# Performance work log

Hardware: AMD Instinct MI355X
Metric: run time of the kernel (lower is better)

Reference implementation:

```python
import jax, jax.numpy as jnp
import numpy as np

NUM_SPECIAL = 3  # rows 1..NUM_SPECIAL in special table; row 0 is padding (zeros)

def setup_inputs() -> dict:
    key = jax.random.key(0)
    ks = jax.random.split(key, 16)
    T, B, E, H, L, V = 128, 32, 512, 512, 2, 32000
    G = 4 * H
    s = 0.02
    special_emb = jax.random.normal(ks[1], (NUM_SPECIAL + 1, E), jnp.float32) * s
    special_emb = special_emb.at[0].set(0.0)  # padding_idx=0
    return {
        "ids": jax.random.randint(ks[0], (T, B), 0, V),
        "length_countdown": jax.random.uniform(ks[2], (T, B, 1), jnp.float32),
        "word_emb": jax.random.normal(ks[3], (V, E), jnp.float32) * s,
        "special_emb": special_emb,
        "h0": jax.random.normal(ks[4], (L, B, H), jnp.float32) * s,
        "c0": jax.random.normal(ks[5], (L, B, H), jnp.float32) * s,
        "prev_output": jnp.zeros((B, H), jnp.float32),
        "Wih0": jax.random.normal(ks[6], (G, E + H + 1), jnp.float32) * s,
        "Whh0": jax.random.normal(ks[7], (G, H), jnp.float32) * s,
        "bih0": jnp.zeros((G,), jnp.float32),
        "bhh0": jnp.zeros((G,), jnp.float32),
        "Wih1": jax.random.normal(ks[8], (G, H), jnp.float32) * s,
        "Whh1": jax.random.normal(ks[9], (G, H), jnp.float32) * s,
        "bih1": jnp.zeros((G,), jnp.float32),
        "bhh1": jnp.zeros((G,), jnp.float32),
        "Wg": jax.random.normal(ks[10], (V, H), jnp.float32) * s,
        "bg": jnp.zeros((V,), jnp.float32),
    }

def _lstm_cell(x, h, c, Wih, Whh, bih, bhh):
    gates = x @ Wih.T + bih + h @ Whh.T + bhh  # [B, 4H]
    i, f, g, o = jnp.split(gates, 4, axis=-1)  # torch LSTMCell gate order
    c_new = jax.nn.sigmoid(f) * c + jax.nn.sigmoid(i) * jnp.tanh(g)
    h_new = jax.nn.sigmoid(o) * jnp.tanh(c_new)
    return h_new, c_new

def reference(ids, length_countdown, word_emb, special_emb, h0, c0, prev_output,
              Wih0, Whh0, bih0, bhh0, Wih1, Whh1, bih1, bhh1, Wg, bg):
    # embeddings = word_embeddings(ids) + special_embeddings(special_ids(ids))
    sp_ids = jnp.where(ids < NUM_SPECIAL, ids + 1, 0)
    emb = word_emb[ids] + special_emb[sp_ids]                 # [T,B,E]
    rnn_in = jnp.concatenate([emb, length_countdown], axis=2)  # [T,B,E+1]

    Wihs = (Wih0, Wih1); Whhs = (Whh0, Whh1)
    bihs = (bih0, bih1); bhhs = (bhh0, bhh1)
    L = h0.shape[0]

    def step(carry, emb_t):
        out, h, c = carry
        x = jnp.concatenate([emb_t, out], axis=1)  # input feeding
        hs, cs = [], []
        for l in range(L):
            h_l, c_l = _lstm_cell(x, h[l], c[l], Wihs[l], Whhs[l], bihs[l], bhhs[l])
            x = h_l  # dropout=0
            hs.append(h_l); cs.append(c_l)
        out = x
        score = jax.nn.log_softmax(out @ Wg.T + bg, axis=-1)  # generator
        return (out, jnp.stack(hs), jnp.stack(cs)), score

    (out, hT, cT), scores = jax.lax.scan(step, (prev_output, h0, c0), rnn_in)
    return scores, (hT, cT), out
```

## Files before the change

kernel.cpp:

```cpp
#include <hip/hip_runtime.h>
#include <hip/hip_bf16.h>


typedef __attribute__((ext_vector_type(8))) short bf16x8;
typedef __attribute__((ext_vector_type(4))) float f32x4;
typedef __attribute__((ext_vector_type(2))) unsigned long long u64x2;

#define AS1 __attribute__((address_space(1)))
#define AS3 __attribute__((address_space(3)))

__device__ __forceinline__ unsigned short f2bf(float f) {
  unsigned int u = __builtin_bit_cast(unsigned int, f);
  u += 0x7fffu + ((u >> 16) & 1u);
  return (unsigned short)(u >> 16);
}

__device__ __forceinline__ void gl16(const void* g, void* l) {
  __builtin_amdgcn_global_load_lds((const AS1 unsigned int*)g,
                                   (AS3 unsigned int*)l, 16, 0, 0);
}

__device__ __forceinline__ float sigm(float x) { return 1.0f / (1.0f + __expf(-x)); }

__global__ __launch_bounds__(256, 1) void prep_k(
    const float* __restrict__ Wg,  const float* __restrict__ Wih0,
    const float* __restrict__ Whh0,const float* __restrict__ Wih1,
    const float* __restrict__ Whh1,const float* __restrict__ bih0,
    const float* __restrict__ bhh0,const float* __restrict__ bih1,
    const float* __restrict__ bhh1,const float* __restrict__ h0,
    const float* __restrict__ pout,
    unsigned short* __restrict__ WgBf, unsigned short* __restrict__ W0e,
    unsigned short* __restrict__ Wr0p, unsigned short* __restrict__ Wr1p,
    float* __restrict__ b1p, float* __restrict__ bias0c,
    float* __restrict__ wcd, unsigned short* __restrict__ H0X,
    unsigned short* __restrict__ FOUT, unsigned short* __restrict__ H1I)
{
  const long N0 = 16384000L;
  const long N1 = N0 + 1048576L;
  const long N2 = N1 + 2097152L;
  const long N3 = N2 + 2097152L;
  const long N4 = N3 + 2048L;
  const long N5 = N4 + 2048L;
  const long N6 = N5 + 2048L;
  const long N7 = N6 + 393216L;
  for (long i = blockIdx.x * 256L + threadIdx.x; i < N7; i += 256L * gridDim.x) {
    if (i < N0) {
      WgBf[i] = f2bf(Wg[i]);
    } else if (i < N1) {
      long k = i - N0; int g = (int)(k >> 9); int kk = (int)(k & 511);
      W0e[k] = f2bf(Wih0[g * 1025 + kk]);
    } else if (i < N2) {
      long k = i - N1; int gp = (int)(k >> 10); int kk = (int)(k & 1023);
      int j = gp >> 2, gate = gp & 3; int g = gate * 512 + j;
      float v = (kk < 512) ? Whh0[g * 512 + kk] : Wih0[g * 1025 + 513 + (kk - 512)];
      Wr0p[k] = f2bf(v);
    } else if (i < N3) {
      long k = i - N2; int gp = (int)(k >> 10); int kk = (int)(k & 1023);
      int j = gp >> 2, gate = gp & 3; int g = gate * 512 + j;
      float v = (kk < 512) ? Wih1[g * 512 + kk] : Whh1[g * 512 + (kk - 512)];
      Wr1p[k] = f2bf(v);
    } else if (i < N4) {
      int gp = (int)(i - N3); int j = gp >> 2, gate = gp & 3; int g = gate * 512 + j;
      b1p[gp] = bih1[g] + bhh1[g];
    } else if (i < N5) {
      int g = (int)(i - N4); bias0c[g] = bih0[g] + bhh0[g];
    } else if (i < N6) {
      int g = (int)(i - N5); wcd[g] = Wih0[g * 1025 + 512];
    } else {
      long k = i - N6;
      int sub = (int)(k / 131072L);
      int e = (int)(k - (long)sub * 131072L);
      int e2 = e & 16383;
      int wgx = e2 >> 9, b = (e2 >> 4) & 31, jl = e2 & 15;
      int j = wgx * 16 + jl;
      float v = (sub == 0) ? h0[b * 512 + j]
              : (sub == 1) ? h0[16384 + b * 512 + j]
                           : pout[b * 512 + j];
      unsigned short* dst = (sub == 0) ? H0X : (sub == 1) ? H1I : FOUT;
      dst[e] = f2bf(v);
    }
  }
}

__global__ __launch_bounds__(256, 1) void emb_k(
    const int* __restrict__ ids, const float* __restrict__ wemb,
    const float* __restrict__ semb, unsigned short* __restrict__ ebf)
{
  const int tb = blockIdx.x;
  const int id = ids[tb];
  const int sp = (id < 3) ? (id + 1) : 0;
  const float* wr = wemb + (long)id * 512;
  const float* sr = semb + sp * 512;
  for (int i = threadIdx.x; i < 512; i += 256)
    ebf[tb * 512 + i] = f2bf(wr[i] + sr[i]);
}

template<int EPI>
__global__ __launch_bounds__(256, 1) void gemm_bt(
    const unsigned short* __restrict__ A,
    const unsigned short* __restrict__ B, int N,
    float* __restrict__ C,
    const float* __restrict__ e0, const float* __restrict__ e1,
    const float* __restrict__ e2)
{
  __shared__ unsigned short sA[4096];
  __shared__ unsigned short sB[4096];
  const int tid = threadIdx.x;
  const int l = tid & 63, w = tid >> 6;
  const int nb = N >> 7;
  const int bid = blockIdx.x;
  const int bm = bid / nb, bn = bid - bm * nb;

  const int u0 = w * 128 + l;
  const int u1 = u0 + 64;
  const int r0 = u0 >> 2, c0 = (u0 & 3) ^ (r0 & 3);
  const int r1 = u1 >> 2, c1 = (u1 & 3) ^ (r1 & 3);
  const unsigned short* ga0 = A + (long)(bm * 128 + r0) * 512 + c0 * 8;
  const unsigned short* ga1 = A + (long)(bm * 128 + r1) * 512 + c1 * 8;
  const unsigned short* gb0 = B + (long)(bn * 128 + r0) * 512 + c0 * 8;
  const unsigned short* gb1 = B + (long)(bn * 128 + r1) * 512 + c1 * 8;
  unsigned short* la0 = sA + (w * 2 + 0) * 512;
  unsigned short* la1 = sA + (w * 2 + 1) * 512;
  unsigned short* lb0 = sB + (w * 2 + 0) * 512;
  unsigned short* lb1 = sB + (w * 2 + 1) * 512;

  const int fr = l & 15, fc = l >> 4;
  const int wm = w >> 1, wn = w & 1;
  int aoff[4], boff[4];
#pragma unroll
  for (int mi = 0; mi < 4; ++mi) {
    int row = wm * 64 + mi * 16 + fr;
    aoff[mi] = row * 64 + ((fc ^ (row & 3)) * 16);
  }
#pragma unroll
  for (int ni = 0; ni < 4; ++ni) {
    int row = wn * 64 + ni * 16 + fr;
    boff[ni] = row * 64 + ((fc ^ (row & 3)) * 16);
  }

  f32x4 acc[4][4];
#pragma unroll
  for (int i = 0; i < 4; ++i)
#pragma unroll
    for (int jq = 0; jq < 4; ++jq) acc[i][jq] = (f32x4){0.f, 0.f, 0.f, 0.f};

  for (int kt = 0; kt < 16; ++kt) {
    __syncthreads();
    gl16(ga0 + kt * 32, la0);
    gl16(ga1 + kt * 32, la1);
    gl16(gb0 + kt * 32, lb0);
    gl16(gb1 + kt * 32, lb1);
    asm volatile("s_waitcnt vmcnt(0)" ::: "memory");
    __syncthreads();
    bf16x8 av[4], bv[4];
#pragma unroll
    for (int mi = 0; mi < 4; ++mi)
      av[mi] = *(const bf16x8*)((const char*)sA + aoff[mi]);
#pragma unroll
    for (int ni = 0; ni < 4; ++ni)
      bv[ni] = *(const bf16x8*)((const char*)sB + boff[ni]);
#pragma unroll
    for (int mi = 0; mi < 4; ++mi)
#pragma unroll
      for (int ni = 0; ni < 4; ++ni)
        acc[mi][ni] = __builtin_amdgcn_mfma_f32_16x16x32_bf16(av[mi], bv[ni], acc[mi][ni], 0, 0, 0);
  }

  const int mbase = bm * 128 + wm * 64;
  const int nbase = bn * 128 + wn * 64;
#pragma unroll
  for (int mi = 0; mi < 4; ++mi)
#pragma unroll
    for (int ni = 0; ni < 4; ++ni) {
      const int col = nbase + ni * 16 + fr;
#pragma unroll
      for (int r = 0; r < 4; ++r) {
        const int row = mbase + mi * 16 + fc * 4 + r;
        float v = acc[mi][ni][r];
        if (EPI == 0) {
          const int gp = ((row & 511) << 2) | (row >> 9);
          v += e0[row] + e2[col] * e1[row];
          C[(long)gp * N + col] = v;
        } else {
          v += e0[col];
          C[(long)row * N + col] = v;
        }
      }
    }
}

__global__ __launch_bounds__(256, 1) void lstm_seq(
    const unsigned short* __restrict__ Wr0p,
    const unsigned short* __restrict__ Wr1p,
    const float* __restrict__ P0t, const float* __restrict__ b1p,
    const float* __restrict__ c0in,
    unsigned short* __restrict__ H0X, unsigned short* __restrict__ H1X,
    const unsigned short* __restrict__ FOUT, const unsigned short* __restrict__ H1I,
    unsigned short* __restrict__ outbf, float* __restrict__ outs,
    unsigned int* __restrict__ flagA, unsigned int* __restrict__ flagB)
{
  const int tid = threadIdx.x;
  const int wg = blockIdx.x;
  const int l = tid & 63, w = tid >> 6;
  const int fr = l & 15, fc = l >> 4;

  __shared__ unsigned short sx[32768];
  __shared__ float sg[32][65];
  __shared__ unsigned short sh[32][16];

  unsigned int xcc;
  asm("s_getreg_b32 %0, hwreg(HW_REG_XCC_ID)" : "=s"(xcc));
  const int eoff = (int)(xcc & 7) << 14;
  const int foff = (int)(xcc & 7) << 10;

  const int b = tid & 31, jl0 = tid >> 5;
  const int sb = l >> 1, sjh = l & 1;

  float c0r[2], c1r[2], h0k[2], h1k[2];
#pragma unroll
  for (int jq = 0; jq < 2; ++jq) {
    c0r[jq] = c0in[b * 512 + wg * 16 + jl0 + jq * 8];
    c1r[jq] = c0in[16384 + b * 512 + wg * 16 + jl0 + jq * 8];
    h0k[jq] = 0.f; h1k[jq] = 0.f;
  }

  float b1v[8];
#pragma unroll
  for (int jq = 0; jq < 2; ++jq)
#pragma unroll
    for (int g = 0; g < 4; ++g)
      b1v[jq * 4 + g] = b1p[(wg * 16 + jl0 + jq * 8) * 4 + g];

  const char* sxb0 = (const char*)sx + fr * 2048;
  const char* sxb1 = (const char*)sx + (16 + fr) * 2048;
  const int xr = (fr & 7) << 4;
  const int wrow = (wg * 64 + w * 16 + fr) * 1024 + fc * 8;

  char* const sxw = (char*)sx + sb * 2048;
  const int sswz = (sb & 7) << 4;

#define STAGE2(srcp, half)                                                    \
  do {                                                                        \
    unsigned long long q0[8], q1[8];                                          \
    _Pragma("unroll")                                                         \
    for (int i = 0; i < 8; ++i) {                                             \
      int u = i * 256 + tid;                                                  \
      q0[i] = __hip_atomic_load((const unsigned long long*)((srcp) + eoff) + u * 2, \
                                __ATOMIC_RELAXED, __HIP_MEMORY_SCOPE_AGENT);  \
      q1[i] = __hip_atomic_load((const unsigned long long*)((srcp) + eoff) + u * 2 + 1, \
                                __ATOMIC_RELAXED, __HIP_MEMORY_SCOPE_AGENT);  \
    }                                                                         \
    _Pragma("unroll")                                                         \
    for (int i = 0; i < 8; ++i) {                                             \
      int cb = (half) * 1024 + (i * 4 + w) * 32 + sjh * 16;                   \
      u64x2 v; v.x = q0[i]; v.y = q1[i];                                      \
      *(u64x2*)(sxw + (cb ^ sswz)) = v;                                       \
    }                                                                         \
  } while (0)

#define MFMA_HALF(Wp, k0, e0v, o0v, e1v, o1v)                                 \
  do {                                                                        \
    _Pragma("unroll")                                                         \
    for (int kp = 0; kp < 8; ++kp) {                                          \
      int kta = (k0) + kp * 2, ktb = kta + 1;                                 \
      bf16x8 bva = *(const bf16x8*)((Wp) + wrow + kta * 32);                  \
      bf16x8 x0a = *(const bf16x8*)(sxb0 + ((kta * 64 + fc * 16) ^ xr));      \
      bf16x8 x1a = *(const bf16x8*)(sxb1 + ((kta * 64 + fc * 16) ^ xr));      \
      e0v = __builtin_amdgcn_mfma_f32_16x16x32_bf16(x0a, bva, e0v, 0, 0, 0);  \
      e1v = __builtin_amdgcn_mfma_f32_16x16x32_bf16(x1a, bva, e1v, 0, 0, 0);  \
      bf16x8 bvb = *(const bf16x8*)((Wp) + wrow + ktb * 32);                  \
      bf16x8 x0b = *(const bf16x8*)(sxb0 + ((ktb * 64 + fc * 16) ^ xr));      \
      bf16x8 x1b = *(const bf16x8*)(sxb1 + ((ktb * 64 + fc * 16) ^ xr));      \
      o0v = __builtin_amdgcn_mfma_f32_16x16x32_bf16(x0b, bvb, o0v, 0, 0, 0);  \
      o1v = __builtin_amdgcn_mfma_f32_16x16x32_bf16(x1b, bvb, o1v, 0, 0, 0);  \
    }                                                                         \
  } while (0)

#define POLL(flags, tgt)                                                      \
  do {                                                                        \
    const unsigned int* fp = (flags) + foff + ((l & 31) << 5);                \
    for (;;) {                                                                \
      unsigned int f = __hip_atomic_load(fp, __ATOMIC_RELAXED,                \
                                         __HIP_MEMORY_SCOPE_AGENT);           \
      if (__all((int)(f >= (unsigned int)(tgt)))) break;                      \
      __builtin_amdgcn_s_sleep(1);                                            \
    }                                                                         \
    asm volatile("" ::: "memory");                                            \
  } while (0)

  STAGE2(H0X, 0);
  __syncthreads();
  if (w == 0 && l < 8)
    __hip_atomic_store(&flagB[l * 1024 + (wg << 5)], 1u,
                       __ATOMIC_RELAXED, __HIP_MEMORY_SCOPE_AGENT);

  for (int t = 0; t < 128; ++t) {
    float p0v[8];
#pragma unroll
    for (int jq = 0; jq < 2; ++jq)
#pragma unroll
      for (int g = 0; g < 4; ++g)
        p0v[jq * 4 + g] =
            P0t[(long)((wg * 16 + jl0 + jq * 8) * 4 + g) * 4096 + t * 32 + b];

    f32x4 aA0e = (f32x4){0.f,0.f,0.f,0.f}, aA0o = (f32x4){0.f,0.f,0.f,0.f};
    f32x4 aA1e = (f32x4){0.f,0.f,0.f,0.f}, aA1o = (f32x4){0.f,0.f,0.f,0.f};
    MFMA_HALF(Wr0p, 0, aA0e, aA0o, aA1e, aA1o);

    POLL(flagB, t + 1);
    if (t == 0) STAGE2(FOUT, 1); else STAGE2(H1X, 1);
    __syncthreads();
    MFMA_HALF(Wr0p, 16, aA0e, aA0o, aA1e, aA1o);
    {
      f32x4 s0 = aA0e + aA0o, s1 = aA1e + aA1o;
#pragma unroll
      for (int r = 0; r < 4; ++r) {
        sg[fc * 4 + r][w * 16 + fr] = s0[r];
        sg[16 + fc * 4 + r][w * 16 + fr] = s1[r];
      }
    }
    __syncthreads();
#pragma unroll
    for (int jq = 0; jq < 2; ++jq) {
      const int jl = jl0 + jq * 8;
      float gi = sg[b][jl * 4 + 0] + p0v[jq * 4 + 0];
      float gf = sg[b][jl * 4 + 1] + p0v[jq * 4 + 1];
      float gg = sg[b][jl * 4 + 2] + p0v[jq * 4 + 2];
      float go = sg[b][jl * 4 + 3] + p0v[jq * 4 + 3];
      float cn = sigm(gf) * c0r[jq] + sigm(gi) * tanhf(gg);
      float hn = sigm(go) * tanhf(cn);
      c0r[jq] = cn; h0k[jq] = hn;
      sh[b][jl] = f2bf(hn);
    }
    __syncthreads();
    if (w == 0) {
      u64x2 v = *(const u64x2*)&sh[sb][sjh * 8];
      unsigned long long* dst0 =
          (unsigned long long*)(H0X + wg * 512 + sb * 16 + sjh * 8);
#pragma unroll
      for (int r = 0; r < 8; ++r) {
        __hip_atomic_store(dst0 + r * 2048,     v.x, __ATOMIC_RELAXED, __HIP_MEMORY_SCOPE_AGENT);
        __hip_atomic_store(dst0 + r * 2048 + 1, v.y, __ATOMIC_RELAXED, __HIP_MEMORY_SCOPE_AGENT);
      }
      asm volatile("s_waitcnt vmcnt(0)" ::: "memory");
      if (l < 8)
        __hip_atomic_store(&flagA[l * 1024 + (wg << 5)], (unsigned int)(t + 1),
                           __ATOMIC_RELAXED, __HIP_MEMORY_SCOPE_AGENT);
    }

    f32x4 aB0e = (f32x4){0.f,0.f,0.f,0.f}, aB0o = (f32x4){0.f,0.f,0.f,0.f};
    f32x4 aB1e = (f32x4){0.f,0.f,0.f,0.f}, aB1o = (f32x4){0.f,0.f,0.f,0.f};
    if (t == 0) {
      STAGE2(H1I, 1);
      __syncthreads();
    }
    MFMA_HALF(Wr1p, 16, aB0e, aB0o, aB1e, aB1o);

    POLL(flagA, t + 1);
    STAGE2(H0X, 0);
    __syncthreads();
    MFMA_HALF(Wr1p, 0, aB0e, aB0o, aB1e, aB1o);
    {
      f32x4 s0 = aB0e + aB0o, s1 = aB1e + aB1o;
#pragma unroll
      for (int r = 0; r < 4; ++r) {
        sg[fc * 4 + r][w * 16 + fr] = s0[r];
        sg[16 + fc * 4 + r][w * 16 + fr] = s1[r];
      }
    }
    __syncthreads();
#pragma unroll
    for (int jq = 0; jq < 2; ++jq) {
      const int jl = jl0 + jq * 8;
      float gi = sg[b][jl * 4 + 0] + b1v[jq * 4 + 0];
      float gf = sg[b][jl * 4 + 1] + b1v[jq * 4 + 1];
      float gg = sg[b][jl * 4 + 2] + b1v[jq * 4 + 2];
      float go = sg[b][jl * 4 + 3] + b1v[jq * 4 + 3];
      float cn = sigm(gf) * c1r[jq] + sigm(gi) * tanhf(gg);
      float hn = sigm(go) * tanhf(cn);
      c1r[jq] = cn; h1k[jq] = hn;
      sh[b][jl] = f2bf(hn);
    }
    __syncthreads();
    if (w == 0) {
      u64x2 v = *(const u64x2*)&sh[sb][sjh * 8];
      unsigned long long* dst0 =
          (unsigned long long*)(H1X + wg * 512 + sb * 16 + sjh * 8);
#pragma unroll
      for (int r = 0; r < 8; ++r) {
        __hip_atomic_store(dst0 + r * 2048,     v.x, __ATOMIC_RELAXED, __HIP_MEMORY_SCOPE_AGENT);
        __hip_atomic_store(dst0 + r * 2048 + 1, v.y, __ATOMIC_RELAXED, __HIP_MEMORY_SCOPE_AGENT);
      }
      asm volatile("s_waitcnt vmcnt(0)" ::: "memory");
      if (l < 8)
        __hip_atomic_store(&flagB[l * 1024 + (wg << 5)], (unsigned int)(t + 2),
                           __ATOMIC_RELAXED, __HIP_MEMORY_SCOPE_AGENT);
    } else if (w == 1) {
      u64x2 v = *(const u64x2*)&sh[sb][sjh * 8];
      *(u64x2*)(outbf + (t * 32 + sb) * 512 + wg * 16 + sjh * 8) = v;
    }
  }
#undef STAGE2
#undef MFMA_HALF
#undef POLL

  float* hT = outs + 131072000;
  float* cT = outs + 131072000 + 32768;
  float* oT = outs + 131072000 + 65536;
#pragma unroll
  for (int jq = 0; jq < 2; ++jq) {
    const int j = wg * 16 + jl0 + jq * 8;
    hT[b * 512 + j] = h0k[jq];
    hT[16384 + b * 512 + j] = h1k[jq];
    cT[b * 512 + j] = c0r[jq];
    cT[16384 + b * 512 + j] = c1r[jq];
    oT[b * 512 + j] = h1k[jq];
  }
}

__global__ __launch_bounds__(256, 1) void lse_fix(float* __restrict__ sc)
{
  const long row = blockIdx.x;
  float4* p4 = (float4*)(sc + row * 32000L);
  const int tid = threadIdx.x;
  float m = -3.0e38f, s = 0.0f;
  for (int i = tid; i < 8000; i += 256) {
    float4 v = p4[i];
    float m4 = fmaxf(fmaxf(v.x, v.y), fmaxf(v.z, v.w));
    float mn = fmaxf(m, m4);
    s = s * __expf(m - mn) + __expf(v.x - mn) + __expf(v.y - mn)
        + __expf(v.z - mn) + __expf(v.w - mn);
    m = mn;
  }
#pragma unroll
  for (int off = 32; off > 0; off >>= 1) {
    float mo = __shfl_down(m, off);
    float so = __shfl_down(s, off);
    float mn = fmaxf(m, mo);
    s = s * __expf(m - mn) + so * __expf(mo - mn);
    m = mn;
  }
  __shared__ float lm[4], ls[4], lse_sh;
  if ((tid & 63) == 0) { lm[tid >> 6] = m; ls[tid >> 6] = s; }
  __syncthreads();
  if (tid == 0) {
    float M = lm[0], S = ls[0];
#pragma unroll
    for (int i = 1; i < 4; ++i) {
      float mn = fmaxf(M, lm[i]);
      S = S * __expf(M - mn) + ls[i] * __expf(lm[i] - mn);
      M = mn;
    }
    lse_sh = M + __logf(S);
  }
  __syncthreads();
  const float lse = lse_sh;
  for (int i = tid; i < 8000; i += 256) {
    float4 v = p4[i];
    v.x -= lse; v.y -= lse; v.z -= lse; v.w -= lse;
    p4[i] = v;
  }
}

extern "C" void kernel_launch(void* const* d_in, const int* in_sizes, int n_in,
                              void* d_out, int out_size, void* d_ws, size_t ws_size,
                              hipStream_t stream) {
  const int*   ids  = (const int*)d_in[0];
  const float* cd   = (const float*)d_in[1];
  const float* wemb = (const float*)d_in[2];
  const float* semb = (const float*)d_in[3];
  const float* h0   = (const float*)d_in[4];
  const float* c0   = (const float*)d_in[5];
  const float* pout = (const float*)d_in[6];
  const float* Wih0 = (const float*)d_in[7];
  const float* Whh0 = (const float*)d_in[8];
  const float* bih0 = (const float*)d_in[9];
  const float* bhh0 = (const float*)d_in[10];
  const float* Wih1 = (const float*)d_in[11];
  const float* Whh1 = (const float*)d_in[12];
  const float* bih1 = (const float*)d_in[13];
  const float* bhh1 = (const float*)d_in[14];
  const float* Wg   = (const float*)d_in[15];
  const float* bg   = (const float*)d_in[16];
  float* out = (float*)d_out;

  char* ws = (char*)d_ws;
  unsigned short* WgBf   = (unsigned short*)(ws);
  unsigned short* W0e    = (unsigned short*)(ws + 32768000);
  unsigned short* Wr0p   = (unsigned short*)(ws + 34865152);
  unsigned short* Wr1p   = (unsigned short*)(ws + 39059456);
  float*          b1p    = (float*)(ws + 43253760);
  float*          bias0c = (float*)(ws + 43261952);
  float*          wcd    = (float*)(ws + 43270144);
  unsigned short* embbf  = (unsigned short*)(ws + 43409408);
  unsigned short* outbf  = (unsigned short*)(ws + 47603712);
  float*          P0t    = (float*)(ws + 51798016);
  unsigned int*   flagA  = (unsigned int*)(ws + 85352448);
  unsigned int*   flagB  = (unsigned int*)(ws + 85385216);
  unsigned short* H0X    = (unsigned short*)(ws + 85417984);
  unsigned short* H1X    = (unsigned short*)(ws + 85680128);
  unsigned short* FOUT   = (unsigned short*)(ws + 85942272);
  unsigned short* H1I    = (unsigned short*)(ws + 86204416);

  hipMemsetAsync((void*)flagA, 0, 65536, stream);

  prep_k<<<8192, 256, 0, stream>>>(Wg, Wih0, Whh0, Wih1, Whh1,
                                   bih0, bhh0, bih1, bhh1, h0, pout,
                                   WgBf, W0e, Wr0p, Wr1p, b1p, bias0c, wcd,
                                   H0X, FOUT, H1I);

  emb_k<<<4096, 256, 0, stream>>>(ids, wemb, semb, embbf);

  gemm_bt<0><<<512, 256, 0, stream>>>(W0e, embbf, 4096, P0t, bias0c, wcd, cd);

  lstm_seq<<<32, 256, 0, stream>>>(Wr0p, Wr1p, P0t, b1p, c0,
                                   H0X, H1X, FOUT, H1I, outbf, out, flagA, flagB);

  gemm_bt<1><<<8000, 256, 0, stream>>>(outbf, WgBf, 32000, out, bg, nullptr, nullptr);

  lse_fix<<<4096, 256, 0, stream>>>(out);
}
```

Baseline: 1.968 ms.

## Tag LSTM hidden exchange with step numbers and fuse softmax partials into GEMM epilogue

Cross-block hidden-state exchange in the persistent LSTM kernel now packs a step tag into the upper 16 bits of each bf16 value. Readers spin until every tag matches, which replaces the separate flag arrays, the waitcnt fences and the per-XCC replicated copies. The generator GEMM epilogue also computes per-tile row max and sum-exp partials, so lse_fix no longer rereads the full 4096x32000 score matrix. The exchange buffers double in size and the spin loop adds block-wide barriers per retry. PMS reuses P0t's workspace region, which is safe only because P0t is dead by then.

```diff
diff --git a/kernel.cpp b/kernel.cpp
--- a/kernel.cpp
+++ b/kernel.cpp
@@ -8,6 +8,8 @@
 
 #define AS1 __attribute__((address_space(1)))
 #define AS3 __attribute__((address_space(3)))
+#define RLX __ATOMIC_RELAXED
+#define AGT __HIP_MEMORY_SCOPE_AGENT
 
 __device__ __forceinline__ unsigned short f2bf(float f) {
   unsigned int u = __builtin_bit_cast(unsigned int, f);
@@ -21,6 +23,14 @@
 }
 
 __device__ __forceinline__ float sigm(float x) { return 1.0f / (1.0f + __expf(-x)); }
+
+__device__ __forceinline__ bool chk2(unsigned long long q, unsigned want) {
+  return (((unsigned)(q >> 16) & 0xffffu) == want) &&
+         (((unsigned)(q >> 48) & 0xffffu) == want);
+}
+__device__ __forceinline__ unsigned pack2(unsigned long long q) {
+  return ((unsigned)q & 0xffffu) | (((unsigned)(q >> 32) & 0xffffu) << 16);
+}
 
 __global__ __launch_bounds__(256, 1) void prep_k(
     const float* __restrict__ Wg,  const float* __restrict__ Wih0,
@@ -32,8 +42,8 @@
     unsigned short* __restrict__ WgBf, unsigned short* __restrict__ W0e,
     unsigned short* __restrict__ Wr0p, unsigned short* __restrict__ Wr1p,
     float* __restrict__ b1p, float* __restrict__ bias0c,
-    float* __restrict__ wcd, unsigned short* __restrict__ H0X,
-    unsigned short* __restrict__ FOUT, unsigned short* __restrict__ H1I)
+    float* __restrict__ wcd, unsigned short* __restrict__ H0I,
+    unsigned short* __restrict__ H1I, unsigned short* __restrict__ FOUT)
 {
   const long N0 = 16384000L;
   const long N1 = N0 + 1048576L;
@@ -42,7 +52,7 @@
   const long N4 = N3 + 2048L;
   const long N5 = N4 + 2048L;
   const long N6 = N5 + 2048L;
-  const long N7 = N6 + 393216L;
+  const long N7 = N6 + 49152L;
   for (long i = blockIdx.x * 256L + threadIdx.x; i < N7; i += 256L * gridDim.x) {
     if (i < N0) {
       WgBf[i] = f2bf(Wg[i]);
@@ -68,15 +78,13 @@
       int g = (int)(i - N5); wcd[g] = Wih0[g * 1025 + 512];
     } else {
       long k = i - N6;
-      int sub = (int)(k / 131072L);
-      int e = (int)(k - (long)sub * 131072L);
-      int e2 = e & 16383;
-      int wgx = e2 >> 9, b = (e2 >> 4) & 31, jl = e2 & 15;
-      int j = wgx * 16 + jl;
+      int sub = (int)(k >> 14);
+      int e = (int)(k & 16383);
+      int b = e >> 9, j = e & 511;
       float v = (sub == 0) ? h0[b * 512 + j]
               : (sub == 1) ? h0[16384 + b * 512 + j]
                            : pout[b * 512 + j];
-      unsigned short* dst = (sub == 0) ? H0X : (sub == 1) ? H1I : FOUT;
+      unsigned short* dst = (sub == 0) ? H0I : (sub == 1) ? H1I : FOUT;
       dst[e] = f2bf(v);
     }
   }
@@ -100,11 +108,12 @@
     const unsigned short* __restrict__ A,
     const unsigned short* __restrict__ B, int N,
     float* __restrict__ C,
-    const float* __restrict__ e0, const float* __restrict__ e1,
+    const float* __restrict__ e0, float* __restrict__ e1,
     const float* __restrict__ e2)
 {
   __shared__ unsigned short sA[4096];
   __shared__ unsigned short sB[4096];
+  __shared__ float pmw[128][2][2];
   const int tid = threadIdx.x;
   const int l = tid & 63, w = tid >> 6;
   const int nb = N >> 7;
@@ -168,25 +177,83 @@
 
   const int mbase = bm * 128 + wm * 64;
   const int nbase = bn * 128 + wn * 64;
-#pragma unroll
-  for (int mi = 0; mi < 4; ++mi)
-#pragma unroll
-    for (int ni = 0; ni < 4; ++ni) {
-      const int col = nbase + ni * 16 + fr;
-#pragma unroll
-      for (int r = 0; r < 4; ++r) {
-        const int row = mbase + mi * 16 + fc * 4 + r;
-        float v = acc[mi][ni][r];
-        if (EPI == 0) {
+
+  if (EPI == 0) {
+#pragma unroll
+    for (int mi = 0; mi < 4; ++mi)
+#pragma unroll
+      for (int ni = 0; ni < 4; ++ni) {
+        const int col = nbase + ni * 16 + fr;
+#pragma unroll
+        for (int r = 0; r < 4; ++r) {
+          const int row = mbase + mi * 16 + fc * 4 + r;
           const int gp = ((row & 511) << 2) | (row >> 9);
-          v += e0[row] + e2[col] * e1[row];
+          float v = acc[mi][ni][r] + e0[row] + e2[col] * e1[row];
           C[(long)gp * N + col] = v;
-        } else {
-          v += e0[col];
-          C[(long)row * N + col] = v;
         }
       }
-    }
+  } else {
+    float m2[4][4], s2[4][4];
+#pragma unroll
+    for (int mi = 0; mi < 4; ++mi)
+#pragma unroll
+      for (int r = 0; r < 4; ++r) { m2[mi][r] = -3.0e38f; s2[mi][r] = 0.f; }
+#pragma unroll
+    for (int mi = 0; mi < 4; ++mi)
+#pragma unroll
+      for (int ni = 0; ni < 4; ++ni) {
+        const int col = nbase + ni * 16 + fr;
+        const float bgc = e0[col];
+#pragma unroll
+        for (int r = 0; r < 4; ++r) {
+          float v = acc[mi][ni][r] + bgc;
+          acc[mi][ni][r] = v;
+          C[(long)(mbase + mi * 16 + fc * 4 + r) * N + col] = v;
+          m2[mi][r] = fmaxf(m2[mi][r], v);
+        }
+      }
+#pragma unroll
+    for (int mi = 0; mi < 4; ++mi)
+#pragma unroll
+      for (int r = 0; r < 4; ++r)
+#pragma unroll
+        for (int s = 1; s < 16; s <<= 1)
+          m2[mi][r] = fmaxf(m2[mi][r], __shfl_xor(m2[mi][r], s));
+#pragma unroll
+    for (int mi = 0; mi < 4; ++mi)
+#pragma unroll
+      for (int ni = 0; ni < 4; ++ni)
+#pragma unroll
+        for (int r = 0; r < 4; ++r)
+          s2[mi][r] += __expf(acc[mi][ni][r] - m2[mi][r]);
+#pragma unroll
+    for (int mi = 0; mi < 4; ++mi)
+#pragma unroll
+      for (int r = 0; r < 4; ++r)
+#pragma unroll
+        for (int s = 1; s < 16; s <<= 1)
+          s2[mi][r] += __shfl_xor(s2[mi][r], s);
+    if (fr == 0) {
+#pragma unroll
+      for (int mi = 0; mi < 4; ++mi)
+#pragma unroll
+        for (int r = 0; r < 4; ++r) {
+          const int rl = wm * 64 + mi * 16 + fc * 4 + r;
+          pmw[rl][wn][0] = m2[mi][r];
+          pmw[rl][wn][1] = s2[mi][r];
+        }
+    }
+    __syncthreads();
+    if (tid < 128) {
+      float ma = pmw[tid][0][0], sa = pmw[tid][0][1];
+      float mb = pmw[tid][1][0], sb = pmw[tid][1][1];
+      float M = fmaxf(ma, mb);
+      float S = sa * __expf(ma - M) + sb * __expf(mb - M);
+      float2* PMS = (float2*)e1;
+      float2 o; o.x = M; o.y = S;
+      PMS[(long)(bm * 128 + tid) * nb + bn] = o;
+    }
+  }
 }
 
 __global__ __launch_bounds__(256, 1) void lstm_seq(
@@ -194,10 +261,10 @@
     const unsigned short* __restrict__ Wr1p,
     const float* __restrict__ P0t, const float* __restrict__ b1p,
     const float* __restrict__ c0in,
-    unsigned short* __restrict__ H0X, unsigned short* __restrict__ H1X,
-    const unsigned short* __restrict__ FOUT, const unsigned short* __restrict__ H1I,
-    unsigned short* __restrict__ outbf, float* __restrict__ outs,
-    unsigned int* __restrict__ flagA, unsigned int* __restrict__ flagB)
+    unsigned int* __restrict__ XH0, unsigned int* __restrict__ XH1,
+    const unsigned short* __restrict__ H0I, const unsigned short* __restrict__ H1I,
+    const unsigned short* __restrict__ FOUT,
+    unsigned short* __restrict__ outbf, float* __restrict__ outs)
 {
   const int tid = threadIdx.x;
   const int wg = blockIdx.x;
@@ -206,15 +273,10 @@
 
   __shared__ unsigned short sx[32768];
   __shared__ float sg[32][65];
-  __shared__ unsigned short sh[32][16];
-
-  unsigned int xcc;
-  asm("s_getreg_b32 %0, hwreg(HW_REG_XCC_ID)" : "=s"(xcc));
-  const int eoff = (int)(xcc & 7) << 14;
-  const int foff = (int)(xcc & 7) << 10;
+  __shared__ unsigned sh[32][16];
+  __shared__ int sBad;
 
   const int b = tid & 31, jl0 = tid >> 5;
-  const int sb = l >> 1, sjh = l & 1;
 
   float c0r[2], c1r[2], h0k[2], h1k[2];
 #pragma unroll
@@ -236,25 +298,54 @@
   const int xr = (fr & 7) << 4;
   const int wrow = (wg * 64 + w * 16 + fr) * 1024 + fc * 8;
 
-  char* const sxw = (char*)sx + sb * 2048;
-  const int sswz = (sb & 7) << 4;
-
-#define STAGE2(srcp, half)                                                    \
+  const int pb = l >> 1, pjh = l & 1;
+
+#define STAGE_INIT(srcp, half)                                                \
   do {                                                                        \
-    unsigned long long q0[8], q1[8];                                          \
     _Pragma("unroll")                                                         \
     for (int i = 0; i < 8; ++i) {                                             \
       int u = i * 256 + tid;                                                  \
-      q0[i] = __hip_atomic_load((const unsigned long long*)((srcp) + eoff) + u * 2, \
-                                __ATOMIC_RELAXED, __HIP_MEMORY_SCOPE_AGENT);  \
-      q1[i] = __hip_atomic_load((const unsigned long long*)((srcp) + eoff) + u * 2 + 1, \
-                                __ATOMIC_RELAXED, __HIP_MEMORY_SCOPE_AGENT);  \
+      u64x2 v = *(const u64x2*)((srcp) + u * 8);                              \
+      int bb = u >> 6, j2 = (u & 63) * 16;                                    \
+      *(u64x2*)((char*)sx + bb * 2048 + ((((half) * 1024) + j2) ^ ((bb & 7) << 4))) = v; \
     }                                                                         \
-    _Pragma("unroll")                                                         \
-    for (int i = 0; i < 8; ++i) {                                             \
-      int cb = (half) * 1024 + (i * 4 + w) * 32 + sjh * 16;                   \
-      u64x2 v; v.x = q0[i]; v.y = q1[i];                                      \
-      *(u64x2*)(sxw + (cb ^ sswz)) = v;                                       \
+  } while (0)
+
+#define STAGE_TAG(srcp, half, want)                                           \
+  do {                                                                        \
+    bool wrote = false;                                                       \
+    for (;;) {                                                                \
+      if (tid == 0) sBad = 0;                                                 \
+      __syncthreads();                                                        \
+      if (!wrote) {                                                           \
+        unsigned long long q[32];                                             \
+        _Pragma("unroll")                                                     \
+        for (int i = 0; i < 16; ++i) {                                        \
+          int u = i * 256 + tid;                                              \
+          q[2*i]   = __hip_atomic_load((const unsigned long long*)(srcp) + u*2,   RLX, AGT); \
+          q[2*i+1] = __hip_atomic_load((const unsigned long long*)(srcp) + u*2+1, RLX, AGT); \
+        }                                                                     \
+        bool all = true;                                                      \
+        _Pragma("unroll")                                                     \
+        for (int i = 0; i < 16; ++i)                                          \
+          all = all && chk2(q[2*i], (want)) && chk2(q[2*i+1], (want));        \
+        if (all) {                                                            \
+          _Pragma("unroll")                                                   \
+          for (int i = 0; i < 16; ++i) {                                      \
+            int u = i * 256 + tid;                                            \
+            int bb = u >> 7, j2 = (u & 127) * 8;                              \
+            unsigned long long v = (unsigned long long)pack2(q[2*i])          \
+                                 | ((unsigned long long)pack2(q[2*i+1]) << 32); \
+            *(unsigned long long*)((char*)sx + bb * 2048                      \
+                 + ((((half) * 1024) + j2) ^ ((bb & 7) << 4))) = v;           \
+          }                                                                   \
+          wrote = true;                                                       \
+        } else {                                                              \
+          sBad = 1;                                                           \
+        }                                                                     \
+      }                                                                       \
+      __syncthreads();                                                        \
+      if (sBad == 0) break;                                                   \
     }                                                                         \
   } while (0)
 
@@ -276,23 +367,8 @@
     }                                                                         \
   } while (0)
 
-#define POLL(flags, tgt)                                                      \
-  do {                                                                        \
-    const unsigned int* fp = (flags) + foff + ((l & 31) << 5);                \
-    for (;;) {                                                                \
-      unsigned int f = __hip_atomic_load(fp, __ATOMIC_RELAXED,                \
-                                         __HIP_MEMORY_SCOPE_AGENT);           \
-      if (__all((int)(f >= (unsigned int)(tgt)))) break;                      \
-      __builtin_amdgcn_s_sleep(1);                                            \
-    }                                                                         \
-    asm volatile("" ::: "memory");                                            \
-  } while (0)
-
-  STAGE2(H0X, 0);
+  STAGE_INIT(H0I, 0);
   __syncthreads();
-  if (w == 0 && l < 8)
-    __hip_atomic_store(&flagB[l * 1024 + (wg << 5)], 1u,
-                       __ATOMIC_RELAXED, __HIP_MEMORY_SCOPE_AGENT);
 
   for (int t = 0; t < 128; ++t) {
     float p0v[8];
@@ -307,9 +383,12 @@
     f32x4 aA1e = (f32x4){0.f,0.f,0.f,0.f}, aA1o = (f32x4){0.f,0.f,0.f,0.f};
     MFMA_HALF(Wr0p, 0, aA0e, aA0o, aA1e, aA1o);
 
-    POLL(flagB, t + 1);
-    if (t == 0) STAGE2(FOUT, 1); else STAGE2(H1X, 1);
-    __syncthreads();
+    if (t == 0) {
+      STAGE_INIT(FOUT, 1);
+      __syncthreads();
+    } else {
+      STAGE_TAG(XH1, 1, (unsigned)(2 * t));
+    }
     MFMA_HALF(Wr0p, 16, aA0e, aA0o, aA1e, aA1o);
     {
       f32x4 s0 = aA0e + aA0o, s1 = aA1e + aA1o;
@@ -320,45 +399,42 @@
       }
     }
     __syncthreads();
-#pragma unroll
-    for (int jq = 0; jq < 2; ++jq) {
-      const int jl = jl0 + jq * 8;
-      float gi = sg[b][jl * 4 + 0] + p0v[jq * 4 + 0];
-      float gf = sg[b][jl * 4 + 1] + p0v[jq * 4 + 1];
-      float gg = sg[b][jl * 4 + 2] + p0v[jq * 4 + 2];
-      float go = sg[b][jl * 4 + 3] + p0v[jq * 4 + 3];
-      float cn = sigm(gf) * c0r[jq] + sigm(gi) * tanhf(gg);
-      float hn = sigm(go) * tanhf(cn);
-      c0r[jq] = cn; h0k[jq] = hn;
-      sh[b][jl] = f2bf(hn);
+    {
+      const unsigned tA = (unsigned)(2 * t + 1) << 16;
+#pragma unroll
+      for (int jq = 0; jq < 2; ++jq) {
+        const int jl = jl0 + jq * 8;
+        float gi = sg[b][jl * 4 + 0] + p0v[jq * 4 + 0];
+        float gf = sg[b][jl * 4 + 1] + p0v[jq * 4 + 1];
+        float gg = sg[b][jl * 4 + 2] + p0v[jq * 4 + 2];
+        float go = sg[b][jl * 4 + 3] + p0v[jq * 4 + 3];
+        float cn = sigm(gf) * c0r[jq] + sigm(gi) * tanhf(gg);
+        float hn = sigm(go) * tanhf(cn);
+        c0r[jq] = cn; h0k[jq] = hn;
+        sh[b][jl] = (unsigned)f2bf(hn) | tA;
+      }
     }
     __syncthreads();
     if (w == 0) {
-      u64x2 v = *(const u64x2*)&sh[sb][sjh * 8];
-      unsigned long long* dst0 =
-          (unsigned long long*)(H0X + wg * 512 + sb * 16 + sjh * 8);
-#pragma unroll
-      for (int r = 0; r < 8; ++r) {
-        __hip_atomic_store(dst0 + r * 2048,     v.x, __ATOMIC_RELAXED, __HIP_MEMORY_SCOPE_AGENT);
-        __hip_atomic_store(dst0 + r * 2048 + 1, v.y, __ATOMIC_RELAXED, __HIP_MEMORY_SCOPE_AGENT);
-      }
-      asm volatile("s_waitcnt vmcnt(0)" ::: "memory");
-      if (l < 8)
-        __hip_atomic_store(&flagA[l * 1024 + (wg << 5)], (unsigned int)(t + 1),
-                           __ATOMIC_RELAXED, __HIP_MEMORY_SCOPE_AGENT);
+      u64x2 v0 = *(const u64x2*)&sh[pb][pjh * 8];
+      u64x2 v1 = *(const u64x2*)&sh[pb][pjh * 8 + 4];
+      unsigned long long* dst =
+          (unsigned long long*)(XH0 + pb * 512 + wg * 16 + pjh * 8);
+      __hip_atomic_store(dst + 0, v0.x, RLX, AGT);
+      __hip_atomic_store(dst + 1, v0.y, RLX, AGT);
+      __hip_atomic_store(dst + 2, v1.x, RLX, AGT);
+      __hip_atomic_store(dst + 3, v1.y, RLX, AGT);
     }
 
     f32x4 aB0e = (f32x4){0.f,0.f,0.f,0.f}, aB0o = (f32x4){0.f,0.f,0.f,0.f};
     f32x4 aB1e = (f32x4){0.f,0.f,0.f,0.f}, aB1o = (f32x4){0.f,0.f,0.f,0.f};
     if (t == 0) {
-      STAGE2(H1I, 1);
+      STAGE_INIT(H1I, 1);
       __syncthreads();
     }
     MFMA_HALF(Wr1p, 16, aB0e, aB0o, aB1e, aB1o);
 
-    POLL(flagA, t + 1);
-    STAGE2(H0X, 0);
-    __syncthreads();
+    STAGE_TAG(XH0, 0, (unsigned)(2 * t + 1));
     MFMA_HALF(Wr1p, 0, aB0e, aB0o, aB1e, aB1o);
     {
       f32x4 s0 = aB0e + aB0o, s1 = aB1e + aB1o;
@@ -369,40 +445,43 @@
       }
     }
     __syncthreads();
-#pragma unroll
-    for (int jq = 0; jq < 2; ++jq) {
-      const int jl = jl0 + jq * 8;
-      float gi = sg[b][jl * 4 + 0] + b1v[jq * 4 + 0];
-      float gf = sg[b][jl * 4 + 1] + b1v[jq * 4 + 1];
-      float gg = sg[b][jl * 4 + 2] + b1v[jq * 4 + 2];
-      float go = sg[b][jl * 4 + 3] + b1v[jq * 4 + 3];
-      float cn = sigm(gf) * c1r[jq] + sigm(gi) * tanhf(gg);
-      float hn = sigm(go) * tanhf(cn);
-      c1r[jq] = cn; h1k[jq] = hn;
-      sh[b][jl] = f2bf(hn);
+    {
+      const unsigned tB = (unsigned)(2 * t + 2) << 16;
+#pragma unroll
+      for (int jq = 0; jq < 2; ++jq) {
+        const int jl = jl0 + jq * 8;
+        float gi = sg[b][jl * 4 + 0] + b1v[jq * 4 + 0];
+        float gf = sg[b][jl * 4 + 1] + b1v[jq * 4 + 1];
+        float gg = sg[b][jl * 4 + 2] + b1v[jq * 4 + 2];
+        float go = sg[b][jl * 4 + 3] + b1v[jq * 4 + 3];
+        float cn = sigm(gf) * c1r[jq] + sigm(gi) * tanhf(gg);
+        float hn = sigm(go) * tanhf(cn);
+        c1r[jq] = cn; h1k[jq] = hn;
+        sh[b][jl] = (unsigned)f2bf(hn) | tB;
+      }
     }
     __syncthreads();
     if (w == 0) {
-      u64x2 v = *(const u64x2*)&sh[sb][sjh * 8];
-      unsigned long long* dst0 =
-          (unsigned long long*)(H1X + wg * 512 + sb * 16 + sjh * 8);
-#pragma unroll
-      for (int r = 0; r < 8; ++r) {
-        __hip_atomic_store(dst0 + r * 2048,     v.x, __ATOMIC_RELAXED, __HIP_MEMORY_SCOPE_AGENT);
-        __hip_atomic_store(dst0 + r * 2048 + 1, v.y, __ATOMIC_RELAXED, __HIP_MEMORY_SCOPE_AGENT);
-      }
-      asm volatile("s_waitcnt vmcnt(0)" ::: "memory");
-      if (l < 8)
-        __hip_atomic_store(&flagB[l * 1024 + (wg << 5)], (unsigned int)(t + 2),
-                           __ATOMIC_RELAXED, __HIP_MEMORY_SCOPE_AGENT);
+      u64x2 v0 = *(const u64x2*)&sh[pb][pjh * 8];
+      u64x2 v1 = *(const u64x2*)&sh[pb][pjh * 8 + 4];
+      unsigned long long* dst =
+          (unsigned long long*)(XH1 + pb * 512 + wg * 16 + pjh * 8);
+      __hip_atomic_store(dst + 0, v0.x, RLX, AGT);
+      __hip_atomic_store(dst + 1, v0.y, RLX, AGT);
+      __hip_atomic_store(dst + 2, v1.x, RLX, AGT);
+      __hip_atomic_store(dst + 3, v1.y, RLX, AGT);
     } else if (w == 1) {
-      u64x2 v = *(const u64x2*)&sh[sb][sjh * 8];
-      *(u64x2*)(outbf + (t * 32 + sb) * 512 + wg * 16 + sjh * 8) = v;
-    }
-  }
-#undef STAGE2
+      const unsigned long long* s = (const unsigned long long*)&sh[pb][pjh * 8];
+      unsigned long long q0 = s[0], q1 = s[1], q2 = s[2], q3 = s[3];
+      u64x2 v;
+      v.x = (unsigned long long)pack2(q0) | ((unsigned long long)pack2(q1) << 32);
+      v.y = (unsigned long long)pack2(q2) | ((unsigned long long)pack2(q3) << 32);
+      *(u64x2*)(outbf + (t * 32 + pb) * 512 + wg * 16 + pjh * 8) = v;
+    }
+  }
+#undef STAGE_INIT
+#undef STAGE_TAG
 #undef MFMA_HALF
-#undef POLL
 
   float* hT = outs + 131072000;
   float* cT = outs + 131072000 + 32768;
@@ -418,19 +497,16 @@
   }
 }
 
-__global__ __launch_bounds__(256, 1) void lse_fix(float* __restrict__ sc)
+__global__ __launch_bounds__(256, 1) void lse_fix(float* __restrict__ sc,
+                                                  const float2* __restrict__ pms)
 {
   const long row = blockIdx.x;
   float4* p4 = (float4*)(sc + row * 32000L);
   const int tid = threadIdx.x;
   float m = -3.0e38f, s = 0.0f;
-  for (int i = tid; i < 8000; i += 256) {
-    float4 v = p4[i];
-    float m4 = fmaxf(fmaxf(v.x, v.y), fmaxf(v.z, v.w));
-    float mn = fmaxf(m, m4);
-    s = s * __expf(m - mn) + __expf(v.x - mn) + __expf(v.y - mn)
-        + __expf(v.z - mn) + __expf(v.w - mn);
-    m = mn;
+  if (tid < 250) {
+    float2 p = pms[row * 250 + tid];
+    m = p.x; s = p.y;
   }
 #pragma unroll
   for (int off = 32; off > 0; off >>= 1) {
@@ -492,31 +568,31 @@
   float*          b1p    = (float*)(ws + 43253760);
   float*          bias0c = (float*)(ws + 43261952);
   float*          wcd    = (float*)(ws + 43270144);
-  unsigned short* embbf  = (unsigned short*)(ws + 43409408);
-  unsigned short* outbf  = (unsigned short*)(ws + 47603712);
-  float*          P0t    = (float*)(ws + 51798016);
-  unsigned int*   flagA  = (unsigned int*)(ws + 85352448);
-  unsigned int*   flagB  = (unsigned int*)(ws + 85385216);
-  unsigned short* H0X    = (unsigned short*)(ws + 85417984);
-  unsigned short* H1X    = (unsigned short*)(ws + 85680128);
-  unsigned short* FOUT   = (unsigned short*)(ws + 85942272);
-  unsigned short* H1I    = (unsigned short*)(ws + 86204416);
-
-  hipMemsetAsync((void*)flagA, 0, 65536, stream);
+  unsigned short* embbf  = (unsigned short*)(ws + 43278336);
+  unsigned short* outbf  = (unsigned short*)(ws + 47472640);
+  float*          P0t    = (float*)(ws + 51666944);
+  float*          PMS    = (float*)(ws + 51666944);
+  unsigned int*   XH0    = (unsigned int*)(ws + 85221376);
+  unsigned int*   XH1    = (unsigned int*)(ws + 85286912);
+  unsigned short* H0I    = (unsigned short*)(ws + 85352448);
+  unsigned short* H1I    = (unsigned short*)(ws + 85385216);
+  unsigned short* FOUT   = (unsigned short*)(ws + 85417984);
+
+  hipMemsetAsync((void*)XH0, 0, 131072, stream);
 
   prep_k<<<8192, 256, 0, stream>>>(Wg, Wih0, Whh0, Wih1, Whh1,
                                    bih0, bhh0, bih1, bhh1, h0, pout,
                                    WgBf, W0e, Wr0p, Wr1p, b1p, bias0c, wcd,
-                                   H0X, FOUT, H1I);
+                                   H0I, H1I, FOUT);
 
   emb_k<<<4096, 256, 0, stream>>>(ids, wemb, semb, embbf);
 
   gemm_bt<0><<<512, 256, 0, stream>>>(W0e, embbf, 4096, P0t, bias0c, wcd, cd);
 
   lstm_seq<<<32, 256, 0, stream>>>(Wr0p, Wr1p, P0t, b1p, c0,
-                                   H0X, H1X, FOUT, H1I, outbf, out, flagA, flagB);
-
-  gemm_bt<1><<<8000, 256, 0, stream>>>(outbf, WgBf, 32000, out, bg, nullptr, nullptr);
-
-  lse_fix<<<4096, 256, 0, stream>>>(out);
-}
+                                   XH0, XH1, H0I, H1I, FOUT, outbf, out);
+
+  gemm_bt<1><<<8000, 256, 0, stream>>>(outbf, WgBf, 32000, out, bg, PMS, nullptr);
+
+  lse_fix<<<4096, 256, 0, stream>>>(out, (const float2*)PMS);
+}
```

Measured after the change: 2.787 ms. 41.6% more time.
